# Optimization experiments

Measured on AMD Instinct MI355X. Metric: run time of the kernel, lower is better.

The kernel has to match this reference:

```python
import jax, jax.numpy as jnp
import numpy as np

D_IN = 64   # T (condition_length)
D = 128     # latent_dim
H = 8       # num_head
N = 2       # batch of graphs
M = 512     # num_nodes
T_OBS = 5.0


def leaky(v):
    return jnp.where(v >= 0, v, 0.2 * v)


def setup_inputs() -> dict:
    key = jax.random.key(0)
    ks = jax.random.split(key, 24)
    g = lambda k, s: jax.random.normal(k, s, dtype=jnp.float32) * 0.05
    return {
        "x": jax.random.normal(ks[0], (N, M, D_IN), dtype=jnp.float32),
        # f_node: T -> 2D -> D
        "fn_w1": g(ks[1], (D_IN, 2 * D)), "fn_b1": g(ks[2], (2 * D,)),
        "fn_w2": g(ks[3], (2 * D, D)),   "fn_b2": g(ks[4], (D,)),
        # per-head K/Q/V projections, stacked over heads
        "wk": g(ks[5], (H, D, D)), "bk": g(ks[6], (H, D)),
        "wq": g(ks[7], (H, D, D)), "bq": g(ks[8], (H, D)),
        "wv": g(ks[9], (H, D, D)), "bv": g(ks[10], (H, D)),
        # f_v: H*D -> D -> D
        "fv_w1": g(ks[11], (H * D, D)), "fv_b1": g(ks[12], (D,)),
        "fv_w2": g(ks[13], (D, D)),     "fv_b2": g(ks[14], (D,)),
        # f_node2edge: 2D -> D -> 1
        "fe_w1": g(ks[15], (2 * D, D)), "fe_b1": g(ks[16], (D,)),
        "fe_w2": g(ks[17], (D, 1)),     "fe_b2": g(ks[18], (1,)),
    }


def reference(x, fn_w1, fn_b1, fn_w2, fn_b2, wk, bk, wq, bq, wv, bv,
              fv_w1, fv_b1, fv_w2, fv_b2, fe_w1, fe_b1, fe_w2, fe_b2):
    n, m, T = x.shape
    # TemporalEncoding with d_hid=1: div_term = [1.0], even col -> sin(t)
    t = jnp.linspace(0.0, T_OBS, T)
    te = jnp.sin(t)  # [T]
    # f_node
    h = jax.nn.relu((x + te) @ fn_w1 + fn_b1) @ fn_w2 + fn_b2  # [N,M,D]
    # per-head attention (sender=K_i, receiver=Q_j -> scores = K Q^T)
    K = jnp.einsum('nmd,hde->hnme', h, wk) + bk[:, None, None, :]
    Q = jnp.einsum('nmd,hde->hnme', h, wq) + bq[:, None, None, :]
    V = jnp.einsum('nmd,hde->hnme', h, wv) + bv[:, None, None, :]
    scores = jnp.einsum('hnid,hnjd->hnij', K, Q)           # [H,N,M,M]
    alpha = jax.nn.softmax(leaky(scores), axis=-1)
    att = leaky(jnp.einsum('hnij,hnjd->hnid', alpha, V))   # [H,N,M,D]
    # concat heads along feature dim (head 0 first)
    att = jnp.transpose(att, (1, 2, 0, 3)).reshape(n, m, -1)  # [N,M,H*D]
    x2 = jax.nn.relu(att @ fv_w1 + fv_b1) @ fv_w2 + fv_b2 + h  # [N,M,D]
    # pairwise node2edge FFN: pair(i,j) = concat(x2_i, x2_j)
    half = fe_w1.shape[0] // 2
    A = x2 @ fe_w1[:half]   # contribution of node i
    B = x2 @ fe_w1[half:]   # contribution of node j
    hid = jax.nn.relu(A[:, :, None, :] + B[:, None, :, :] + fe_b1)  # [N,M,M,D]
    edge = (hid @ fe_w2 + fe_b2)[..., 0] / float(m)  # [N,M,M]
    return (x2, edge)
```

## Files before the change

### kernel.cpp

```cpp
#include <hip/hip_runtime.h>

typedef unsigned short u16;
typedef unsigned int u32;
typedef __attribute__((ext_vector_type(8))) short short8;
typedef __attribute__((ext_vector_type(4))) float f32x4;

__device__ __forceinline__ u16 f2b(float f) {
  union { float f; u32 i; } v; v.f = f;
  u32 i = v.i;
  return (u16)((i + 0x7FFFu + ((i >> 16) & 1u)) >> 16);
}
__device__ __forceinline__ float lo16(u32 x) { union { u32 i; float f; } v; v.i = x << 16; return v.f; }
__device__ __forceinline__ float hi16(u32 x) { union { u32 i; float f; } v; v.i = x & 0xffff0000u; return v.f; }
__device__ __forceinline__ u32 pack2(float a, float b) { return (u32)f2b(a) | ((u32)f2b(b) << 16); }

__device__ __align__(16) float g_h[1024 * 128];
__device__ __align__(16) u16   g_hb[1024 * 128];
__device__ __align__(16) u16   g_Wt[24 * 128 * 128];
__device__ __align__(16) u16   g_w1t[128 * 1024];
__device__ __align__(16) u16   g_w2t[128 * 128];
__device__ __align__(16) u16   g_fat[2 * 128 * 128];
__device__ __align__(16) u16   g_Opb[512 * 64 * 128];
__device__ __align__(16) float g_ml[512 * 64 * 2];
__device__ __align__(16) float g_A[1024 * 128];
__device__ __align__(16) float g_Bm[1024 * 128];

__global__ void k_fnode(const float* __restrict__ x, const float* __restrict__ w1,
                        const float* __restrict__ b1, const float* __restrict__ w2,
                        const float* __restrict__ b2, const float* __restrict__ wk,
                        const float* __restrict__ wq, const float* __restrict__ wv,
                        const float* __restrict__ fvw1, const float* __restrict__ fvw2,
                        const float* __restrict__ few1) {
  __shared__ float xr[2 * 64];
  __shared__ float hids[2 * 256];
  __shared__ float red[2048];
  int tx = threadIdx.x;
  int row0 = blockIdx.x * 2;
  if (tx < 128) {
    int r = tx >> 6, k = tx & 63;
    xr[tx] = x[(row0 + r) * 64 + k] + sinf((float)k * (5.0f / 63.0f));
  }
  {
    int base = blockIdx.x * 1280 + tx;
#pragma unroll
    for (int t = 0; t < 5; t++) {
      int idx = base + t * 256;
      if (idx < 393216) {
        int ph = idx >> 14, rem = idx & 16383, e = rem >> 7, d = rem & 127;
        int proj = ph >> 3, head = ph & 7;
        const float* W = (proj == 0) ? wk : (proj == 1) ? wq : wv;
        g_Wt[idx] = f2b(W[head * 16384 + d * 128 + e]);
      } else if (idx < 524288) {
        int idx2 = idx - 393216;
        int e = idx2 >> 10, k = idx2 & 1023;
        g_w1t[idx2] = f2b(fvw1[k * 128 + e]);
      } else if (idx < 540672) {
        int idx3 = idx - 524288;
        int e = idx3 >> 7, k = idx3 & 127;
        g_w2t[idx3] = f2b(fvw2[k * 128 + e]);
      } else if (idx < 573440) {
        int idx4 = idx - 540672;
        int half = idx4 >> 14, rem = idx4 & 16383;
        int e = rem >> 7, k = rem & 127;
        g_fat[idx4] = f2b(few1[(half * 128 + k) * 128 + e]);
      }
    }
  }
  __syncthreads();
  {
    int ks = tx >> 6, cg = tx & 63;
    float acc[2][4] = {};
#pragma unroll 4
    for (int i = 0; i < 16; i++) {
      int k = ks * 16 + i;
      float4 w4 = *(const float4*)&w1[k * 256 + cg * 4];
      float a0 = xr[k], a1 = xr[64 + k];
      acc[0][0] = fmaf(a0, w4.x, acc[0][0]); acc[0][1] = fmaf(a0, w4.y, acc[0][1]);
      acc[0][2] = fmaf(a0, w4.z, acc[0][2]); acc[0][3] = fmaf(a0, w4.w, acc[0][3]);
      acc[1][0] = fmaf(a1, w4.x, acc[1][0]); acc[1][1] = fmaf(a1, w4.y, acc[1][1]);
      acc[1][2] = fmaf(a1, w4.z, acc[1][2]); acc[1][3] = fmaf(a1, w4.w, acc[1][3]);
    }
#pragma unroll
    for (int r = 0; r < 2; r++)
      *(float4*)&red[ks * 512 + r * 256 + cg * 4] = *(float4*)acc[r];
  }
  __syncthreads();
#pragma unroll
  for (int jo = 0; jo < 2; jo++) {
    int o = jo * 256 + tx;
    float s = red[o] + red[512 + o] + red[1024 + o] + red[1536 + o];
    hids[o] = fmaxf(s + b1[o & 255], 0.0f);
  }
  __syncthreads();
  {
    int ks = tx >> 5, eg = tx & 31;
    float acc[2][4] = {};
#pragma unroll 4
    for (int i = 0; i < 32; i++) {
      int k = ks * 32 + i;
      float4 w4 = *(const float4*)&w2[k * 128 + eg * 4];
      float a0 = hids[k], a1 = hids[256 + k];
      acc[0][0] = fmaf(a0, w4.x, acc[0][0]); acc[0][1] = fmaf(a0, w4.y, acc[0][1]);
      acc[0][2] = fmaf(a0, w4.z, acc[0][2]); acc[0][3] = fmaf(a0, w4.w, acc[0][3]);
      acc[1][0] = fmaf(a1, w4.x, acc[1][0]); acc[1][1] = fmaf(a1, w4.y, acc[1][1]);
      acc[1][2] = fmaf(a1, w4.z, acc[1][2]); acc[1][3] = fmaf(a1, w4.w, acc[1][3]);
    }
    __syncthreads();
#pragma unroll
    for (int r = 0; r < 2; r++)
      *(float4*)&red[ks * 256 + r * 128 + eg * 4] = *(float4*)acc[r];
  }
  __syncthreads();
  {
    float s = 0.0f;
#pragma unroll
    for (int ks = 0; ks < 8; ks++) s += red[ks * 256 + tx];
    int r = tx >> 7, e = tx & 127;
    float v = s + b2[e];
    g_h[(row0 + r) * 128 + e] = v;
    g_hb[(row0 + r) * 128 + e] = f2b(v);
  }
}

__global__ __launch_bounds__(256) void k_qattn(
    const float* __restrict__ bk, const float* __restrict__ bq,
    const float* __restrict__ bv) {
  __shared__ u16 RW[128 * 136];
  __shared__ u16 Qs[64 * 136];
  __shared__ u16 Vt[128 * 72];
  u16* Ks = RW;
  u16* Pw = RW;
  float* alphas = (float*)&RW[16384];

  int b = blockIdx.x, tx = threadIdx.x;
  int jc = b & 3, it = (b >> 2) & 7, hn = b >> 5;
  int head = hn >> 1, n = hn & 1;
  int i0 = it * 64;
  int lane = tx & 63, wv = tx >> 6, cl = lane & 15, quad = lane >> 4;
  const u16* WtK = g_Wt + head * 16384;
  const u16* WtQ = g_Wt + (8 + head) * 16384;
  const u16* WtV = g_Wt + (16 + head) * 16384;
  f32x4 zero = {0.0f, 0.0f, 0.0f, 0.0f};

#pragma unroll
  for (int t = 0; t < 8; t++) {
    int idx = t * 256 + tx, row = idx >> 4, oct = idx & 15;
    *(uint4*)&RW[row * 136 + oct * 8] = *(const uint4*)&WtK[row * 128 + oct * 8];
  }
  __syncthreads();
  {
    const u16* hbK = &g_hb[(n * 512 + i0 + wv * 16 + cl) * 128];
    short8 bH[4];
#pragma unroll
    for (int kk = 0; kk < 4; kk++)
      bH[kk] = *(const short8*)&hbK[kk * 32 + quad * 8];
    f32x4 acc[8];
#pragma unroll
    for (int em = 0; em < 8; em++) acc[em] = zero;
#pragma unroll
    for (int em = 0; em < 8; em++)
#pragma unroll
      for (int kk = 0; kk < 4; kk++) {
        short8 aW = *(const short8*)&RW[(em * 16 + cl) * 136 + kk * 32 + quad * 8];
        acc[em] = __builtin_amdgcn_mfma_f32_16x16x32_bf16(aW, bH[kk], acc[em], 0, 0, 0);
      }
    __syncthreads();
#pragma unroll
    for (int em = 0; em < 8; em++) {
      float4 b4 = *(const float4*)&bk[head * 128 + em * 16 + quad * 4];
      int addr = (wv * 16 + cl) * 136 + em * 16 + quad * 4;
      *(u32*)&Ks[addr] = pack2(acc[em][0] + b4.x, acc[em][1] + b4.y);
      *(u32*)&Ks[addr + 2] = pack2(acc[em][2] + b4.z, acc[em][3] + b4.w);
    }
  }
  __syncthreads();
  short8 bK[4];
#pragma unroll
  for (int kk = 0; kk < 4; kk++)
    bK[kk] = *(const short8*)&Ks[(wv * 16 + cl) * 136 + kk * 32 + quad * 8];

  f32x4 o[8];
#pragma unroll
  for (int es = 0; es < 8; es++) o[es] = zero;
  float m_ = -1e30f, l_ = 0.0f;

  for (int jt = 0; jt < 2; jt++) {
    int j0 = jc * 128 + jt * 64;
    __syncthreads();
    const u16* hbJ = &g_hb[(n * 512 + j0 + wv * 16 + cl) * 128];
    short8 bH[4];
#pragma unroll
    for (int kk = 0; kk < 4; kk++)
      bH[kk] = *(const short8*)&hbJ[kk * 32 + quad * 8];
#pragma unroll
    for (int t = 0; t < 8; t++) {
      int idx = t * 256 + tx, row = idx >> 4, oct = idx & 15;
      *(uint4*)&RW[row * 136 + oct * 8] = *(const uint4*)&WtQ[row * 128 + oct * 8];
    }
    __syncthreads();
    {
      f32x4 acc[8];
#pragma unroll
      for (int em = 0; em < 8; em++) acc[em] = zero;
#pragma unroll
      for (int em = 0; em < 8; em++)
#pragma unroll
        for (int kk = 0; kk < 4; kk++) {
          short8 aW = *(const short8*)&RW[(em * 16 + cl) * 136 + kk * 32 + quad * 8];
          acc[em] = __builtin_amdgcn_mfma_f32_16x16x32_bf16(aW, bH[kk], acc[em], 0, 0, 0);
        }
#pragma unroll
      for (int em = 0; em < 8; em++) {
        float4 b4 = *(const float4*)&bq[head * 128 + em * 16 + quad * 4];
        int addr = (wv * 16 + cl) * 136 + em * 16 + quad * 4;
        *(u32*)&Qs[addr] = pack2(acc[em][0] + b4.x, acc[em][1] + b4.y);
        *(u32*)&Qs[addr + 2] = pack2(acc[em][2] + b4.z, acc[em][3] + b4.w);
      }
    }
    __syncthreads();
#pragma unroll
    for (int t = 0; t < 8; t++) {
      int idx = t * 256 + tx, row = idx >> 4, oct = idx & 15;
      *(uint4*)&RW[row * 136 + oct * 8] = *(const uint4*)&WtV[row * 128 + oct * 8];
    }
    __syncthreads();
    {
      f32x4 acc[8];
#pragma unroll
      for (int em = 0; em < 8; em++) acc[em] = zero;
#pragma unroll
      for (int em = 0; em < 8; em++)
#pragma unroll
        for (int kk = 0; kk < 4; kk++) {
          short8 aW = *(const short8*)&RW[(em * 16 + cl) * 136 + kk * 32 + quad * 8];
          acc[em] = __builtin_amdgcn_mfma_f32_16x16x32_bf16(aW, bH[kk], acc[em], 0, 0, 0);
        }
      int jl = wv * 16 + cl;
#pragma unroll
      for (int em = 0; em < 8; em++) {
        float4 b4 = *(const float4*)&bv[head * 128 + em * 16 + quad * 4];
        Vt[(em * 16 + quad * 4 + 0) * 72 + jl] = f2b(acc[em][0] + b4.x);
        Vt[(em * 16 + quad * 4 + 1) * 72 + jl] = f2b(acc[em][1] + b4.y);
        Vt[(em * 16 + quad * 4 + 2) * 72 + jl] = f2b(acc[em][2] + b4.z);
        Vt[(em * 16 + quad * 4 + 3) * 72 + jl] = f2b(acc[em][3] + b4.w);
      }
    }
    __syncthreads();
    f32x4 st[4];
#pragma unroll
    for (int s = 0; s < 4; s++) {
      f32x4 acc = zero;
#pragma unroll
      for (int kk = 0; kk < 4; kk++) {
        short8 aQ = *(const short8*)&Qs[(s * 16 + cl) * 136 + kk * 32 + quad * 8];
        acc = __builtin_amdgcn_mfma_f32_16x16x32_bf16(aQ, bK[kk], acc, 0, 0, 0);
      }
      st[s] = acc;
    }
    float p[4][4];
    float tm = -1e30f;
#pragma unroll
    for (int s = 0; s < 4; s++)
#pragma unroll
      for (int r = 0; r < 4; r++) {
        float v = st[s][r];
        v = fmaxf(v, 0.2f * v);
        p[s][r] = v;
        tm = fmaxf(tm, v);
      }
    tm = fmaxf(tm, __shfl_xor(tm, 16));
    tm = fmaxf(tm, __shfl_xor(tm, 32));
    float mn = fmaxf(m_, tm);
    float alpha = __expf(m_ - mn);
    m_ = mn;
    float ps = 0.0f;
#pragma unroll
    for (int s = 0; s < 4; s++)
#pragma unroll
      for (int r = 0; r < 4; r++) {
        float e = __expf(p[s][r] - mn);
        p[s][r] = e;
        ps += e;
      }
    ps += __shfl_xor(ps, 16);
    ps += __shfl_xor(ps, 32);
    l_ = l_ * alpha + ps;
#pragma unroll
    for (int s = 0; s < 4; s++) {
      uint2 w2v = make_uint2(pack2(p[s][0], p[s][1]), pack2(p[s][2], p[s][3]));
      *(uint2*)&Pw[(wv * 16 + cl) * 72 + s * 16 + quad * 4] = w2v;
    }
    if (quad == 0) alphas[wv * 16 + cl] = alpha;
    __syncthreads();
    f32x4 av = *(const f32x4*)&alphas[wv * 16 + quad * 4];
#pragma unroll
    for (int es = 0; es < 8; es++) o[es] *= av;
    short8 aP[2];
#pragma unroll
    for (int k2 = 0; k2 < 2; k2++)
      aP[k2] = *(const short8*)&Pw[(wv * 16 + cl) * 72 + k2 * 32 + quad * 8];
#pragma unroll
    for (int es = 0; es < 8; es++) {
#pragma unroll
      for (int k2 = 0; k2 < 2; k2++) {
        short8 bV = *(const short8*)&Vt[(es * 16 + cl) * 72 + k2 * 32 + quad * 8];
        o[es] = __builtin_amdgcn_mfma_f32_16x16x32_bf16(aP[k2], bV, o[es], 0, 0, 0);
      }
    }
  }
#pragma unroll
  for (int es = 0; es < 8; es++)
#pragma unroll
    for (int r = 0; r < 4; r++)
      g_Opb[(b * 64 + wv * 16 + quad * 4 + r) * 128 + es * 16 + cl] = f2b(o[es][r]);
  if (quad == 0) {
    g_ml[(b * 64 + wv * 16 + cl) * 2 + 0] = m_;
    g_ml[(b * 64 + wv * 16 + cl) * 2 + 1] = l_;
  }
}

__global__ __launch_bounds__(512) void k_fv(
    const float* __restrict__ fv_b1, const float* __restrict__ fv_b2,
    const float* __restrict__ fe_b1, float* __restrict__ x2out) {
  __shared__ u16 atts[16 * 1032];
  __shared__ u16 wst[128 * 136];
  __shared__ u16 hidb[16 * 136];
  __shared__ u16 x2b[16 * 136];
  int b = blockIdx.x, tx = threadIdx.x;
  int r0 = b * 16;

  {
    int task = tx >> 2, q4 = tx & 3;
    int lr = task >> 3, head = task & 7;
    int gr = r0 + lr;
    int n = gr >> 9, i = gr & 511;
    int it = i >> 6, lr64 = i & 63;
    int hn = head * 2 + n;
    int mlbase = (hn * 32 + it * 4) * 64 + lr64;
    float mc[4], lc[4];
#pragma unroll
    for (int c = 0; c < 4; c++) {
      float2 ml = *(const float2*)&g_ml[(mlbase + c * 64) * 2];
      mc[c] = ml.x; lc[c] = ml.y;
    }
    float ms = fmaxf(fmaxf(mc[0], mc[1]), fmaxf(mc[2], mc[3]));
    float lsum = 0.0f;
    float ra[32];
#pragma unroll
    for (int i2 = 0; i2 < 32; i2++) ra[i2] = 0.0f;
#pragma unroll
    for (int c = 0; c < 4; c++) {
      float w = __expf(mc[c] - ms);
      lsum += w * lc[c];
      const u16* src = &g_Opb[(mlbase + c * 64) * 128 + q4 * 32];
#pragma unroll
      for (int ov = 0; ov < 4; ov++) {
        uint4 v = *(const uint4*)&src[ov * 8];
        ra[ov * 8 + 0] = fmaf(w, lo16(v.x), ra[ov * 8 + 0]);
        ra[ov * 8 + 1] = fmaf(w, hi16(v.x), ra[ov * 8 + 1]);
        ra[ov * 8 + 2] = fmaf(w, lo16(v.y), ra[ov * 8 + 2]);
        ra[ov * 8 + 3] = fmaf(w, hi16(v.y), ra[ov * 8 + 3]);
        ra[ov * 8 + 4] = fmaf(w, lo16(v.z), ra[ov * 8 + 4]);
        ra[ov * 8 + 5] = fmaf(w, hi16(v.z), ra[ov * 8 + 5]);
        ra[ov * 8 + 6] = fmaf(w, lo16(v.w), ra[ov * 8 + 6]);
        ra[ov * 8 + 7] = fmaf(w, hi16(v.w), ra[ov * 8 + 7]);
      }
    }
    float inv = 1.0f / lsum;
    u32 pk[16];
#pragma unroll
    for (int i2 = 0; i2 < 16; i2++) {
      float v0 = ra[i2 * 2] * inv;     v0 = fmaxf(v0, 0.2f * v0);
      float v1 = ra[i2 * 2 + 1] * inv; v1 = fmaxf(v1, 0.2f * v1);
      pk[i2] = pack2(v0, v1);
    }
    int dst = lr * 1032 + head * 128 + q4 * 32;
#pragma unroll
    for (int ov = 0; ov < 4; ov++)
      *(uint4*)&atts[dst + ov * 8] =
          make_uint4(pk[ov * 4], pk[ov * 4 + 1], pk[ov * 4 + 2], pk[ov * 4 + 3]);
  }
  __syncthreads();

  int lane = tx & 63, w = tx >> 6, cl = lane & 15, quad = lane >> 4;
  f32x4 zero = {0.0f, 0.0f, 0.0f, 0.0f};

  f32x4 accH = zero;
  for (int kc = 0; kc < 8; kc++) {
#pragma unroll
    for (int t = 0; t < 4; t++) {
      int idx = t * 512 + tx, row = idx >> 4, oct = idx & 15;
      *(uint4*)&wst[row * 136 + oct * 8] =
          *(const uint4*)&g_w1t[row * 1024 + kc * 128 + oct * 8];
    }
    __syncthreads();
    short8 bA[4];
#pragma unroll
    for (int kk = 0; kk < 4; kk++)
      bA[kk] = *(const short8*)&atts[cl * 1032 + kc * 128 + kk * 32 + quad * 8];
#pragma unroll
    for (int kk = 0; kk < 4; kk++) {
      short8 aW = *(const short8*)&wst[(w * 16 + cl) * 136 + kk * 32 + quad * 8];
      accH = __builtin_amdgcn_mfma_f32_16x16x32_bf16(aW, bA[kk], accH, 0, 0, 0);
    }
    __syncthreads();
  }
  {
    int eb = w * 16 + quad * 4;
    float4 b4 = *(const float4*)&fv_b1[eb];
    float v0 = fmaxf(accH[0] + b4.x, 0.0f);
    float v1 = fmaxf(accH[1] + b4.y, 0.0f);
    float v2 = fmaxf(accH[2] + b4.z, 0.0f);
    float v3 = fmaxf(accH[3] + b4.w, 0.0f);
    *(u32*)&hidb[cl * 136 + eb] = pack2(v0, v1);
    *(u32*)&hidb[cl * 136 + eb + 2] = pack2(v2, v3);
  }
#pragma unroll
  for (int t = 0; t < 4; t++) {
    int idx = t * 512 + tx, row = idx >> 4, oct = idx & 15;
    *(uint4*)&wst[row * 136 + oct * 8] = *(const uint4*)&g_w2t[row * 128 + oct * 8];
  }
  __syncthreads();
  {
    short8 bH2[4];
#pragma unroll
    for (int kk = 0; kk < 4; kk++)
      bH2[kk] = *(const short8*)&hidb[cl * 136 + kk * 32 + quad * 8];
    int gr = r0 + cl;
    f32x4 acc2 = zero;
#pragma unroll
    for (int kk = 0; kk < 4; kk++) {
      short8 aW = *(const short8*)&wst[(w * 16 + cl) * 136 + kk * 32 + quad * 8];
      acc2 = __builtin_amdgcn_mfma_f32_16x16x32_bf16(aW, bH2[kk], acc2, 0, 0, 0);
    }
    int eb = w * 16 + quad * 4;
    float4 b4 = *(const float4*)&fv_b2[eb];
    float4 h4 = *(const float4*)&g_h[gr * 128 + eb];
    float4 xv;
    xv.x = acc2[0] + b4.x + h4.x;
    xv.y = acc2[1] + b4.y + h4.y;
    xv.z = acc2[2] + b4.z + h4.z;
    xv.w = acc2[3] + b4.w + h4.w;
    *(float4*)&x2out[gr * 128 + eb] = xv;
    *(u32*)&x2b[cl * 136 + eb] = pack2(xv.x, xv.y);
    *(u32*)&x2b[cl * 136 + eb + 2] = pack2(xv.z, xv.w);
  }
  __syncthreads();
#pragma unroll
  for (int t = 0; t < 4; t++) {
    int idx = t * 512 + tx, row = idx >> 4, oct = idx & 15;
    *(uint4*)&wst[row * 136 + oct * 8] = *(const uint4*)&g_fat[row * 128 + oct * 8];
  }
  __syncthreads();
  short8 bX[4];
#pragma unroll
  for (int kk = 0; kk < 4; kk++)
    bX[kk] = *(const short8*)&x2b[cl * 136 + kk * 32 + quad * 8];
  {
    int gr = r0 + cl;
    f32x4 accA = zero;
#pragma unroll
    for (int kk = 0; kk < 4; kk++) {
      short8 aW = *(const short8*)&wst[(w * 16 + cl) * 136 + kk * 32 + quad * 8];
      accA = __builtin_amdgcn_mfma_f32_16x16x32_bf16(aW, bX[kk], accA, 0, 0, 0);
    }
    int eb = w * 16 + quad * 4;
    float4 b4 = *(const float4*)&fe_b1[eb];
    float4 av;
    av.x = accA[0] + b4.x; av.y = accA[1] + b4.y;
    av.z = accA[2] + b4.z; av.w = accA[3] + b4.w;
    *(float4*)&g_A[gr * 128 + eb] = av;
  }
  __syncthreads();
#pragma unroll
  for (int t = 0; t < 4; t++) {
    int idx = t * 512 + tx, row = idx >> 4, oct = idx & 15;
    *(uint4*)&wst[row * 136 + oct * 8] =
        *(const uint4*)&g_fat[16384 + row * 128 + oct * 8];
  }
  __syncthreads();
  {
    int gr = r0 + cl;
    f32x4 accB = zero;
#pragma unroll
    for (int kk = 0; kk < 4; kk++) {
      short8 aW = *(const short8*)&wst[(w * 16 + cl) * 136 + kk * 32 + quad * 8];
      accB = __builtin_amdgcn_mfma_f32_16x16x32_bf16(aW, bX[kk], accB, 0, 0, 0);
    }
    int eb = w * 16 + quad * 4;
    *(f32x4*)&g_Bm[gr * 128 + eb] = accB;
  }
}

__global__ void k_edge(const float* __restrict__ few2, const float* __restrict__ feb2,
                       float* __restrict__ edge) {
  __shared__ float As[4 * 128];
  __shared__ float w2s[128];
  int b = blockIdx.x, tx = threadIdx.x;
  int n = b >> 8, rest = b & 255, ig = rest >> 1, jh = rest & 1;
  int i0 = ig * 4;
  if (tx < 128) w2s[tx] = few2[tx];
  As[tx] = g_A[(n * 512 + i0) * 128 + tx];
  As[tx + 256] = g_A[(n * 512 + i0) * 128 + tx + 256];
  float eb2 = feb2[0];
  __syncthreads();
  int j = jh * 256 + tx;
  const float* B0 = &g_Bm[(n * 512 + j) * 128];
  float acc[4] = {};
#pragma unroll 4
  for (int dc = 0; dc < 32; dc++) {
    float4 bv = *(const float4*)&B0[dc * 4];
    float4 w4 = *(const float4*)&w2s[dc * 4];
#pragma unroll
    for (int i = 0; i < 4; i++) {
      float4 a4 = *(const float4*)&As[i * 128 + dc * 4];
      acc[i] = fmaf(fmaxf(a4.x + bv.x, 0.0f), w4.x, acc[i]);
      acc[i] = fmaf(fmaxf(a4.y + bv.y, 0.0f), w4.y, acc[i]);
      acc[i] = fmaf(fmaxf(a4.z + bv.z, 0.0f), w4.z, acc[i]);
      acc[i] = fmaf(fmaxf(a4.w + bv.w, 0.0f), w4.w, acc[i]);
    }
  }
  const float scale = 1.0f / 512.0f;
#pragma unroll
  for (int i = 0; i < 4; i++)
    edge[(n * 512 + i0 + i) * 512 + j] = (acc[i] + eb2) * scale;
}

extern "C" void kernel_launch(void* const* d_in, const int* in_sizes, int n_in,
                              void* d_out, int out_size, void* d_ws, size_t ws_size,
                              hipStream_t stream) {
  (void)in_sizes; (void)n_in; (void)out_size; (void)d_ws; (void)ws_size;
  const float* x     = (const float*)d_in[0];
  const float* fn_w1 = (const float*)d_in[1];
  const float* fn_b1 = (const float*)d_in[2];
  const float* fn_w2 = (const float*)d_in[3];
  const float* fn_b2 = (const float*)d_in[4];
  const float* wk    = (const float*)d_in[5];
  const float* bk    = (const float*)d_in[6];
  const float* wq    = (const float*)d_in[7];
  const float* bq    = (const float*)d_in[8];
  const float* wv    = (const float*)d_in[9];
  const float* bv    = (const float*)d_in[10];
  const float* fv_w1 = (const float*)d_in[11];
  const float* fv_b1 = (const float*)d_in[12];
  const float* fv_w2 = (const float*)d_in[13];
  const float* fv_b2 = (const float*)d_in[14];
  const float* fe_w1 = (const float*)d_in[15];
  const float* fe_b1 = (const float*)d_in[16];
  const float* fe_w2 = (const float*)d_in[17];
  const float* fe_b2 = (const float*)d_in[18];

  float* x2out = (float*)d_out;
  float* edge  = x2out + 131072;

  k_fnode<<<512, 256, 0, stream>>>(x, fn_w1, fn_b1, fn_w2, fn_b2, wk, wq, wv,
                                   fv_w1, fv_w2, fe_w1);
  k_qattn<<<512, 256, 0, stream>>>(bk, bq, bv);
  k_fv<<<64, 512, 0, stream>>>(fv_b1, fv_b2, fe_b1, x2out);
  k_edge<<<512, 256, 0, stream>>>(fe_w2, fe_b2, edge);
}
```

Measured before the change: 148.3 us.

## Merge two i-tiles per attention block and register-prefetch weights in k_fv

k_qattn now runs 256 blocks of 512 threads, each covering two 64-row i-tiles. The Q and V projection weights staged in shared memory are shared by both tiles, and the Q/V projection output columns are split across the two wave groups, which halves per-tile weight staging and projection work. k_fv prefetches the next weight chunk into registers while the current chunk is consumed, overlapping global loads with MFMA. The trade-off is fewer blocks on the GPU, more threads per block, and higher register pressure.

```diff
diff --git a/kernel.cpp b/kernel.cpp
--- a/kernel.cpp
+++ b/kernel.cpp
@@ -122,34 +122,35 @@
   }
 }
 
-__global__ __launch_bounds__(256) void k_qattn(
+__global__ __launch_bounds__(512) void k_qattn(
     const float* __restrict__ bk, const float* __restrict__ bq,
     const float* __restrict__ bv) {
   __shared__ u16 RW[128 * 136];
   __shared__ u16 Qs[64 * 136];
   __shared__ u16 Vt[128 * 72];
-  u16* Ks = RW;
-  u16* Pw = RW;
-  float* alphas = (float*)&RW[16384];
+  float* alphas = (float*)&RW[9216];
 
   int b = blockIdx.x, tx = threadIdx.x;
-  int jc = b & 3, it = (b >> 2) & 7, hn = b >> 5;
+  int jc = b & 3, itp = (b >> 2) & 3, hn = b >> 4;
   int head = hn >> 1, n = hn & 1;
+  int lane = tx & 63, wv = tx >> 6;
+  int itl = wv >> 2, wvl = wv & 3;
+  int it = itp * 2 + itl;
   int i0 = it * 64;
-  int lane = tx & 63, wv = tx >> 6, cl = lane & 15, quad = lane >> 4;
+  int cl = lane & 15, quad = lane >> 4;
   const u16* WtK = g_Wt + head * 16384;
   const u16* WtQ = g_Wt + (8 + head) * 16384;
   const u16* WtV = g_Wt + (16 + head) * 16384;
   f32x4 zero = {0.0f, 0.0f, 0.0f, 0.0f};
 
 #pragma unroll
-  for (int t = 0; t < 8; t++) {
-    int idx = t * 256 + tx, row = idx >> 4, oct = idx & 15;
+  for (int t = 0; t < 4; t++) {
+    int idx = t * 512 + tx, row = idx >> 4, oct = idx & 15;
     *(uint4*)&RW[row * 136 + oct * 8] = *(const uint4*)&WtK[row * 128 + oct * 8];
   }
   __syncthreads();
   {
-    const u16* hbK = &g_hb[(n * 512 + i0 + wv * 16 + cl) * 128];
+    const u16* hbK = &g_hb[(n * 512 + i0 + wvl * 16 + cl) * 128];
     short8 bH[4];
 #pragma unroll
     for (int kk = 0; kk < 4; kk++)
@@ -168,16 +169,16 @@
 #pragma unroll
     for (int em = 0; em < 8; em++) {
       float4 b4 = *(const float4*)&bk[head * 128 + em * 16 + quad * 4];
-      int addr = (wv * 16 + cl) * 136 + em * 16 + quad * 4;
-      *(u32*)&Ks[addr] = pack2(acc[em][0] + b4.x, acc[em][1] + b4.y);
-      *(u32*)&Ks[addr + 2] = pack2(acc[em][2] + b4.z, acc[em][3] + b4.w);
+      int addr = (itl * 64 + wvl * 16 + cl) * 136 + em * 16 + quad * 4;
+      *(u32*)&RW[addr] = pack2(acc[em][0] + b4.x, acc[em][1] + b4.y);
+      *(u32*)&RW[addr + 2] = pack2(acc[em][2] + b4.z, acc[em][3] + b4.w);
     }
   }
   __syncthreads();
   short8 bK[4];
 #pragma unroll
   for (int kk = 0; kk < 4; kk++)
-    bK[kk] = *(const short8*)&Ks[(wv * 16 + cl) * 136 + kk * 32 + quad * 8];
+    bK[kk] = *(const short8*)&RW[(itl * 64 + wvl * 16 + cl) * 136 + kk * 32 + quad * 8];
 
   f32x4 o[8];
 #pragma unroll
@@ -187,62 +188,64 @@
   for (int jt = 0; jt < 2; jt++) {
     int j0 = jc * 128 + jt * 64;
     __syncthreads();
-    const u16* hbJ = &g_hb[(n * 512 + j0 + wv * 16 + cl) * 128];
+    const u16* hbJ = &g_hb[(n * 512 + j0 + wvl * 16 + cl) * 128];
     short8 bH[4];
 #pragma unroll
     for (int kk = 0; kk < 4; kk++)
       bH[kk] = *(const short8*)&hbJ[kk * 32 + quad * 8];
 #pragma unroll
-    for (int t = 0; t < 8; t++) {
-      int idx = t * 256 + tx, row = idx >> 4, oct = idx & 15;
+    for (int t = 0; t < 4; t++) {
+      int idx = t * 512 + tx, row = idx >> 4, oct = idx & 15;
       *(uint4*)&RW[row * 136 + oct * 8] = *(const uint4*)&WtQ[row * 128 + oct * 8];
     }
     __syncthreads();
     {
-      f32x4 acc[8];
-#pragma unroll
-      for (int em = 0; em < 8; em++) acc[em] = zero;
-#pragma unroll
-      for (int em = 0; em < 8; em++)
+      f32x4 a4[4];
+#pragma unroll
+      for (int e2 = 0; e2 < 4; e2++) a4[e2] = zero;
+#pragma unroll
+      for (int e2 = 0; e2 < 4; e2++)
 #pragma unroll
         for (int kk = 0; kk < 4; kk++) {
-          short8 aW = *(const short8*)&RW[(em * 16 + cl) * 136 + kk * 32 + quad * 8];
-          acc[em] = __builtin_amdgcn_mfma_f32_16x16x32_bf16(aW, bH[kk], acc[em], 0, 0, 0);
+          short8 aW = *(const short8*)&RW[((itl * 4 + e2) * 16 + cl) * 136 + kk * 32 + quad * 8];
+          a4[e2] = __builtin_amdgcn_mfma_f32_16x16x32_bf16(aW, bH[kk], a4[e2], 0, 0, 0);
         }
 #pragma unroll
-      for (int em = 0; em < 8; em++) {
+      for (int e2 = 0; e2 < 4; e2++) {
+        int em = itl * 4 + e2;
         float4 b4 = *(const float4*)&bq[head * 128 + em * 16 + quad * 4];
-        int addr = (wv * 16 + cl) * 136 + em * 16 + quad * 4;
-        *(u32*)&Qs[addr] = pack2(acc[em][0] + b4.x, acc[em][1] + b4.y);
-        *(u32*)&Qs[addr + 2] = pack2(acc[em][2] + b4.z, acc[em][3] + b4.w);
-      }
-    }
-    __syncthreads();
-#pragma unroll
-    for (int t = 0; t < 8; t++) {
-      int idx = t * 256 + tx, row = idx >> 4, oct = idx & 15;
+        int addr = (wvl * 16 + cl) * 136 + em * 16 + quad * 4;
+        *(u32*)&Qs[addr] = pack2(a4[e2][0] + b4.x, a4[e2][1] + b4.y);
+        *(u32*)&Qs[addr + 2] = pack2(a4[e2][2] + b4.z, a4[e2][3] + b4.w);
+      }
+    }
+    __syncthreads();
+#pragma unroll
+    for (int t = 0; t < 4; t++) {
+      int idx = t * 512 + tx, row = idx >> 4, oct = idx & 15;
       *(uint4*)&RW[row * 136 + oct * 8] = *(const uint4*)&WtV[row * 128 + oct * 8];
     }
     __syncthreads();
     {
-      f32x4 acc[8];
-#pragma unroll
-      for (int em = 0; em < 8; em++) acc[em] = zero;
-#pragma unroll
-      for (int em = 0; em < 8; em++)
+      f32x4 v4[4];
+#pragma unroll
+      for (int e2 = 0; e2 < 4; e2++) v4[e2] = zero;
+#pragma unroll
+      for (int e2 = 0; e2 < 4; e2++)
 #pragma unroll
         for (int kk = 0; kk < 4; kk++) {
-          short8 aW = *(const short8*)&RW[(em * 16 + cl) * 136 + kk * 32 + quad * 8];
-          acc[em] = __builtin_amdgcn_mfma_f32_16x16x32_bf16(aW, bH[kk], acc[em], 0, 0, 0);
+          short8 aW = *(const short8*)&RW[((itl * 4 + e2) * 16 + cl) * 136 + kk * 32 + quad * 8];
+          v4[e2] = __builtin_amdgcn_mfma_f32_16x16x32_bf16(aW, bH[kk], v4[e2], 0, 0, 0);
         }
-      int jl = wv * 16 + cl;
-#pragma unroll
-      for (int em = 0; em < 8; em++) {
+      int jl = wvl * 16 + cl;
+#pragma unroll
+      for (int e2 = 0; e2 < 4; e2++) {
+        int em = itl * 4 + e2;
         float4 b4 = *(const float4*)&bv[head * 128 + em * 16 + quad * 4];
-        Vt[(em * 16 + quad * 4 + 0) * 72 + jl] = f2b(acc[em][0] + b4.x);
-        Vt[(em * 16 + quad * 4 + 1) * 72 + jl] = f2b(acc[em][1] + b4.y);
-        Vt[(em * 16 + quad * 4 + 2) * 72 + jl] = f2b(acc[em][2] + b4.z);
-        Vt[(em * 16 + quad * 4 + 3) * 72 + jl] = f2b(acc[em][3] + b4.w);
+        Vt[(em * 16 + quad * 4 + 0) * 72 + jl] = f2b(v4[e2][0] + b4.x);
+        Vt[(em * 16 + quad * 4 + 1) * 72 + jl] = f2b(v4[e2][1] + b4.y);
+        Vt[(em * 16 + quad * 4 + 2) * 72 + jl] = f2b(v4[e2][2] + b4.z);
+        Vt[(em * 16 + quad * 4 + 3) * 72 + jl] = f2b(v4[e2][3] + b4.w);
       }
     }
     __syncthreads();
@@ -288,17 +291,17 @@
 #pragma unroll
     for (int s = 0; s < 4; s++) {
       uint2 w2v = make_uint2(pack2(p[s][0], p[s][1]), pack2(p[s][2], p[s][3]));
-      *(uint2*)&Pw[(wv * 16 + cl) * 72 + s * 16 + quad * 4] = w2v;
-    }
-    if (quad == 0) alphas[wv * 16 + cl] = alpha;
-    __syncthreads();
-    f32x4 av = *(const f32x4*)&alphas[wv * 16 + quad * 4];
+      *(uint2*)&RW[(itl * 64 + wvl * 16 + cl) * 72 + s * 16 + quad * 4] = w2v;
+    }
+    if (quad == 0) alphas[itl * 64 + wvl * 16 + cl] = alpha;
+    __syncthreads();
+    f32x4 av = *(const f32x4*)&alphas[itl * 64 + wvl * 16 + quad * 4];
 #pragma unroll
     for (int es = 0; es < 8; es++) o[es] *= av;
     short8 aP[2];
 #pragma unroll
     for (int k2 = 0; k2 < 2; k2++)
-      aP[k2] = *(const short8*)&Pw[(wv * 16 + cl) * 72 + k2 * 32 + quad * 8];
+      aP[k2] = *(const short8*)&RW[(itl * 64 + wvl * 16 + cl) * 72 + k2 * 32 + quad * 8];
 #pragma unroll
     for (int es = 0; es < 8; es++) {
 #pragma unroll
@@ -308,14 +311,15 @@
       }
     }
   }
+  int vb = hn * 32 + it * 4 + jc;
 #pragma unroll
   for (int es = 0; es < 8; es++)
 #pragma unroll
     for (int r = 0; r < 4; r++)
-      g_Opb[(b * 64 + wv * 16 + quad * 4 + r) * 128 + es * 16 + cl] = f2b(o[es][r]);
+      g_Opb[(vb * 64 + wvl * 16 + quad * 4 + r) * 128 + es * 16 + cl] = f2b(o[es][r]);
   if (quad == 0) {
-    g_ml[(b * 64 + wv * 16 + cl) * 2 + 0] = m_;
-    g_ml[(b * 64 + wv * 16 + cl) * 2 + 1] = l_;
+    g_ml[(vb * 64 + wvl * 16 + cl) * 2 + 0] = m_;
+    g_ml[(vb * 64 + wvl * 16 + cl) * 2 + 1] = l_;
   }
 }
 
@@ -328,6 +332,12 @@
   __shared__ u16 x2b[16 * 136];
   int b = blockIdx.x, tx = threadIdx.x;
   int r0 = b * 16;
+  int srow[4], soct[4];
+#pragma unroll
+  for (int t = 0; t < 4; t++) {
+    int idx = t * 512 + tx;
+    srow[t] = idx >> 4; soct[t] = idx & 15;
+  }
 
   {
     int task = tx >> 2, q4 = tx & 3;
@@ -380,20 +390,30 @@
       *(uint4*)&atts[dst + ov * 8] =
           make_uint4(pk[ov * 4], pk[ov * 4 + 1], pk[ov * 4 + 2], pk[ov * 4 + 3]);
   }
-  __syncthreads();
 
   int lane = tx & 63, w = tx >> 6, cl = lane & 15, quad = lane >> 4;
   f32x4 zero = {0.0f, 0.0f, 0.0f, 0.0f};
 
+  uint4 rg[4];
+#pragma unroll
+  for (int t = 0; t < 4; t++)
+    rg[t] = *(const uint4*)&g_w1t[srow[t] * 1024 + soct[t] * 8];
   f32x4 accH = zero;
   for (int kc = 0; kc < 8; kc++) {
-#pragma unroll
-    for (int t = 0; t < 4; t++) {
-      int idx = t * 512 + tx, row = idx >> 4, oct = idx & 15;
-      *(uint4*)&wst[row * 136 + oct * 8] =
-          *(const uint4*)&g_w1t[row * 1024 + kc * 128 + oct * 8];
-    }
-    __syncthreads();
+    __syncthreads();
+#pragma unroll
+    for (int t = 0; t < 4; t++)
+      *(uint4*)&wst[srow[t] * 136 + soct[t] * 8] = rg[t];
+    __syncthreads();
+    if (kc < 7) {
+#pragma unroll
+      for (int t = 0; t < 4; t++)
+        rg[t] = *(const uint4*)&g_w1t[srow[t] * 1024 + (kc + 1) * 128 + soct[t] * 8];
+    } else {
+#pragma unroll
+      for (int t = 0; t < 4; t++)
+        rg[t] = *(const uint4*)&g_w2t[srow[t] * 128 + soct[t] * 8];
+    }
     short8 bA[4];
 #pragma unroll
     for (int kk = 0; kk < 4; kk++)
@@ -403,7 +423,6 @@
       short8 aW = *(const short8*)&wst[(w * 16 + cl) * 136 + kk * 32 + quad * 8];
       accH = __builtin_amdgcn_mfma_f32_16x16x32_bf16(aW, bA[kk], accH, 0, 0, 0);
     }
-    __syncthreads();
   }
   {
     int eb = w * 16 + quad * 4;
@@ -415,12 +434,14 @@
     *(u32*)&hidb[cl * 136 + eb] = pack2(v0, v1);
     *(u32*)&hidb[cl * 136 + eb + 2] = pack2(v2, v3);
   }
-#pragma unroll
-  for (int t = 0; t < 4; t++) {
-    int idx = t * 512 + tx, row = idx >> 4, oct = idx & 15;
-    *(uint4*)&wst[row * 136 + oct * 8] = *(const uint4*)&g_w2t[row * 128 + oct * 8];
-  }
-  __syncthreads();
+  __syncthreads();
+#pragma unroll
+  for (int t = 0; t < 4; t++)
+    *(uint4*)&wst[srow[t] * 136 + soct[t] * 8] = rg[t];
+  __syncthreads();
+#pragma unroll
+  for (int t = 0; t < 4; t++)
+    rg[t] = *(const uint4*)&g_fat[srow[t] * 128 + soct[t] * 8];
   {
     short8 bH2[4];
 #pragma unroll
@@ -447,11 +468,12 @@
   }
   __syncthreads();
 #pragma unroll
-  for (int t = 0; t < 4; t++) {
-    int idx = t * 512 + tx, row = idx >> 4, oct = idx & 15;
-    *(uint4*)&wst[row * 136 + oct * 8] = *(const uint4*)&g_fat[row * 128 + oct * 8];
-  }
-  __syncthreads();
+  for (int t = 0; t < 4; t++)
+    *(uint4*)&wst[srow[t] * 136 + soct[t] * 8] = rg[t];
+  __syncthreads();
+#pragma unroll
+  for (int t = 0; t < 4; t++)
+    rg[t] = *(const uint4*)&g_fat[16384 + srow[t] * 128 + soct[t] * 8];
   short8 bX[4];
 #pragma unroll
   for (int kk = 0; kk < 4; kk++)
@@ -473,11 +495,8 @@
   }
   __syncthreads();
 #pragma unroll
-  for (int t = 0; t < 4; t++) {
-    int idx = t * 512 + tx, row = idx >> 4, oct = idx & 15;
-    *(uint4*)&wst[row * 136 + oct * 8] =
-        *(const uint4*)&g_fat[16384 + row * 128 + oct * 8];
-  }
+  for (int t = 0; t < 4; t++)
+    *(uint4*)&wst[srow[t] * 136 + soct[t] * 8] = rg[t];
   __syncthreads();
   {
     int gr = r0 + cl;
@@ -555,7 +574,7 @@
 
   k_fnode<<<512, 256, 0, stream>>>(x, fn_w1, fn_b1, fn_w2, fn_b2, wk, wq, wv,
                                    fv_w1, fv_w2, fe_w1);
-  k_qattn<<<512, 256, 0, stream>>>(bk, bq, bv);
+  k_qattn<<<256, 512, 0, stream>>>(bk, bq, bv);
   k_fv<<<64, 512, 0, stream>>>(fv_b1, fv_b2, fe_b1, x2out);
   k_edge<<<512, 256, 0, stream>>>(fe_w2, fe_b2, edge);
 }
```

Result: slower. 159.6 us (+7.6%).
